# Kernel tuning notes

Hardware: AMD Instinct MI355X
Metric: run time of the kernel (lower is better)

## Reference

```python
import jax, jax.numpy as jnp
import numpy as np

B, T, U = 8, 200, 50
EPROJS = 512
DUNITS = 512
EMB = 512
JOINT = 512
ODIM = 1000
BLANK = 0


def setup_inputs() -> dict:
    key = jax.random.key(0)
    ks = jax.random.split(key, 16)
    s = lambda k, shape: (jax.random.normal(k, shape, jnp.float32) * 0.05)
    inp = {
        "hs_pad": jax.random.normal(ks[0], (B, T, EPROJS), jnp.float32),
        "ys_in_pad": jax.random.randint(ks[1], (B, U), 0, ODIM),
        "emb": s(ks[2], (ODIM, EMB)),
        "W_ih_0": s(ks[3], (4 * DUNITS, EMB)),
        "W_hh_0": s(ks[4], (4 * DUNITS, DUNITS)),
        "b_ih_0": s(ks[5], (4 * DUNITS,)),
        "b_hh_0": s(ks[6], (4 * DUNITS,)),
        "W_ih_1": s(ks[7], (4 * DUNITS, DUNITS)),
        "W_hh_1": s(ks[8], (4 * DUNITS, DUNITS)),
        "b_ih_1": s(ks[9], (4 * DUNITS,)),
        "b_hh_1": s(ks[10], (4 * DUNITS,)),
        "W_enc": s(ks[11], (JOINT, EPROJS)),
        "b_enc": s(ks[12], (JOINT,)),
        "W_dec": s(ks[13], (JOINT, DUNITS)),
        "W_out": s(ks[14], (ODIM, JOINT)),
        "b_out": s(ks[15], (ODIM,)),
    }
    return inp


def _lstm_cell(x, h, c, W_ih, W_hh, b_ih, b_hh):
    # torch.nn.LSTMCell, gate order i, f, g, o
    gates = x @ W_ih.T + b_ih + h @ W_hh.T + b_hh
    i, f, g, o = jnp.split(gates, 4, axis=-1)
    c_new = jax.nn.sigmoid(f) * c + jax.nn.sigmoid(i) * jnp.tanh(g)
    h_new = jax.nn.sigmoid(o) * jnp.tanh(c_new)
    return h_new, c_new


def reference(hs_pad, ys_in_pad, emb, W_ih_0, W_hh_0, b_ih_0, b_hh_0,
              W_ih_1, W_hh_1, b_ih_1, b_hh_1, W_enc, b_enc, W_dec,
              W_out, b_out):
    # embedding with padding_idx=blank -> blank row is zero
    emb_tbl = emb.at[BLANK].set(0.0)
    eys = emb_tbl[ys_in_pad]            # (B, U, EMB)

    def step(carry, ey):
        h0, c0, h1, c1 = carry
        h0, c0 = _lstm_cell(ey, h0, c0, W_ih_0, W_hh_0, b_ih_0, b_hh_0)
        h1, c1 = _lstm_cell(h0, h1, c1, W_ih_1, W_hh_1, b_ih_1, b_hh_1)
        return (h0, c0, h1, c1), h1

    z0 = jnp.zeros((hs_pad.shape[0], DUNITS), hs_pad.dtype)
    _, h_dec = jax.lax.scan(step, (z0, z0, z0, z0),
                            jnp.swapaxes(eys, 0, 1))   # (U, B, D)
    h_dec = jnp.swapaxes(h_dec, 0, 1)                  # (B, U, D)

    # joint: project first, then broadcast-add (avoids (B,T,U,Henc) expand)
    z_enc = hs_pad @ W_enc.T + b_enc                   # (B, T, J)
    z_dec = h_dec @ W_dec.T                            # (B, U, J), no bias
    z = jnp.tanh(z_enc[:, :, None, :] + z_dec[:, None, :, :])  # (B,T,U,J)
    return z @ W_out.T + b_out                         # (B, T, U, ODIM)
```

## Files before the change

kernel.cpp:

```cpp
#include <hip/hip_runtime.h>
#include <cstdint>
#include <cstddef>

#define Tsz 200
#define Usz 50
#define Kd  512
#define G4h 2048
#define OD  1000

typedef __attribute__((ext_vector_type(8))) short short8;
typedef __attribute__((ext_vector_type(4))) short s16x4;
typedef __attribute__((ext_vector_type(4))) float f32x4;

__device__ __forceinline__ unsigned short f2bf(float x) {
  union { float f; unsigned u; } v; v.f = x;
  unsigned r = v.u + 0x7FFFu + ((v.u >> 16) & 1u);
  return (unsigned short)(r >> 16);
}
__device__ __forceinline__ float bf2f(unsigned short h) {
  union { unsigned u; float f; } v; v.u = ((unsigned)h) << 16; return v.f;
}
__device__ __forceinline__ void splits(float w, short& hi, short& lo) {
  unsigned short h = f2bf(w);
  hi = (short)h;
  lo = (short)f2bf(w - bf2f(h));
}
__device__ __forceinline__ void split8(float4 f0, float4 f1, short8& hi, short8& lo) {
  float v[8] = {f0.x, f0.y, f0.z, f0.w, f1.x, f1.y, f1.z, f1.w};
  #pragma unroll
  for (int i = 0; i < 8; ++i) { short a, b2; splits(v[i], a, b2); hi[i] = a; lo[i] = b2; }
}
__device__ __forceinline__ float ftanh(float x) {
  float ax = fabsf(x);
  float t = __expf(-2.0f * ax);
  float r = (1.0f - t) / (1.0f + t);
  return copysignf(r, x);
}
__device__ __forceinline__ float sigf(float x) {
  return 1.0f / (1.0f + __expf(-x));
}
__device__ __forceinline__ void astore(unsigned* p, unsigned v) {
  __hip_atomic_store(p, v, __ATOMIC_RELAXED, __HIP_MEMORY_SCOPE_AGENT);
}
__device__ __forceinline__ void gload16(const void* g, void* l) {
  __builtin_amdgcn_global_load_lds(
      (const __attribute__((address_space(1))) void*)g,
      (__attribute__((address_space(3))) void*)l, 16, 0, 0);
}
__device__ __forceinline__ void aload4x4(const unsigned* p0, const unsigned* p1,
                                         const unsigned* p2, const unsigned* p3,
                                         uint4& r0, uint4& r1, uint4& r2, uint4& r3) {
  asm volatile(
      "global_load_dwordx4 %0, %4, off sc0 sc1\n\t"
      "global_load_dwordx4 %1, %5, off sc0 sc1\n\t"
      "global_load_dwordx4 %2, %6, off sc0 sc1\n\t"
      "global_load_dwordx4 %3, %7, off sc0 sc1\n\t"
      "s_waitcnt vmcnt(0)"
      : "=&v"(r0), "=&v"(r1), "=&v"(r2), "=&v"(r3)
      : "v"(p0), "v"(p1), "v"(p2), "v"(p3)
      : "memory");
}
__device__ __forceinline__ void aload8x4(const unsigned* p0, const unsigned* p1,
                                         const unsigned* p2, const unsigned* p3,
                                         const unsigned* q0, const unsigned* q1,
                                         const unsigned* q2, const unsigned* q3,
                                         uint4& r0, uint4& r1, uint4& r2, uint4& r3,
                                         uint4& s0, uint4& s1, uint4& s2, uint4& s3) {
  asm volatile(
      "global_load_dwordx4 %0, %8, off sc0 sc1\n\t"
      "global_load_dwordx4 %1, %9, off sc0 sc1\n\t"
      "global_load_dwordx4 %2, %10, off sc0 sc1\n\t"
      "global_load_dwordx4 %3, %11, off sc0 sc1\n\t"
      "global_load_dwordx4 %4, %12, off sc0 sc1\n\t"
      "global_load_dwordx4 %5, %13, off sc0 sc1\n\t"
      "global_load_dwordx4 %6, %14, off sc0 sc1\n\t"
      "global_load_dwordx4 %7, %15, off sc0 sc1\n\t"
      "s_waitcnt vmcnt(0)"
      : "=&v"(r0), "=&v"(r1), "=&v"(r2), "=&v"(r3),
        "=&v"(s0), "=&v"(s1), "=&v"(s2), "=&v"(s3)
      : "v"(p0), "v"(p1), "v"(p2), "v"(p3),
        "v"(q0), "v"(q1), "v"(q2), "v"(q3)
      : "memory");
}
__device__ __forceinline__ unsigned tagbad4(uint4 v, unsigned tg) {
  return ((v.x ^ tg) | (v.y ^ tg) | (v.z ^ tg) | (v.w ^ tg)) & 0xFFu;
}

__global__ __launch_bounds__(256) void k_prep(
    const int* __restrict__ ys, const float* __restrict__ emb,
    const float* __restrict__ Wih0, const float* __restrict__ bih0,
    const float* __restrict__ bhh0,
    unsigned* __restrict__ h0s, unsigned* __restrict__ h1s,
    float* __restrict__ xgr) {
  __shared__ float Al[16 * 516];
  __shared__ int idxs[16];
  const int bid = blockIdx.x;
  const int tid = threadIdx.x;

  if (bid < 16) {
    int i = bid * 256 + tid;
    if (i < 4096) { h0s[i] = 0u; h1s[i] = 0u; }
    return;
  }
  int q = bid - 16;
  int m0 = (q % 25) * 16;
  int n0 = (q / 25) * 64;
  if (tid < 16) {
    int m = m0 + tid;
    int u = m >> 3, b = m & 7;
    idxs[tid] = ys[b * Usz + u];
  }
  __syncthreads();
  for (int i = tid; i < 16 * 512; i += 256) {
    int r = i >> 9, k = i & 511;
    int idx = idxs[r];
    Al[r * 516 + k] = (idx == 0) ? 0.0f : emb[(size_t)idx * Kd + k];
  }
  __syncthreads();
  int nl = tid & 63;
  int mg = (tid >> 6) * 4;
  int n = n0 + nl;
  const float* Wr = Wih0 + (size_t)n * Kd;
  float acc[4] = {0.f, 0.f, 0.f, 0.f};
  #pragma unroll 4
  for (int k = 0; k < 512; k += 4) {
    float4 w = *(const float4*)(Wr + k);
    #pragma unroll
    for (int j = 0; j < 4; ++j) {
      const float* ar = &Al[(mg + j) * 516 + k];
      acc[j] += ar[0] * w.x + ar[1] * w.y + ar[2] * w.z + ar[3] * w.w;
    }
  }
  float bias = bih0[n] + bhh0[n];
  int g = n >> 9, jc = n & 511;
  #pragma unroll
  for (int j = 0; j < 4; ++j) {
    int m = m0 + mg + j;
    int u = m >> 3, b = m & 7;
    xgr[(((size_t)u * 32 + (jc >> 4)) * 4 + g) * 128 + (jc & 15) * 8 + b] =
        acc[j] + bias;
  }
}

__global__ __launch_bounds__(256) void k_gemm(const float* __restrict__ A,
                                              const float* __restrict__ W,
                                              float* __restrict__ C, int N) {
  __shared__ float Al[16 * 516];
  int m0 = blockIdx.x * 16;
  int n0 = blockIdx.y * 64;
  for (int i = threadIdx.x; i < 16 * 512; i += 256) {
    int r = i >> 9, k = i & 511;
    Al[r * 516 + k] = A[(size_t)(m0 + r) * Kd + k];
  }
  __syncthreads();
  int nl = threadIdx.x & 63;
  int mg = (threadIdx.x >> 6) * 4;
  int n = n0 + nl;
  const float* Wr = W + (size_t)n * Kd;
  float acc[4] = {0.f, 0.f, 0.f, 0.f};
  #pragma unroll 4
  for (int k = 0; k < 512; k += 4) {
    float4 w = *(const float4*)(Wr + k);
    #pragma unroll
    for (int j = 0; j < 4; ++j) {
      const float* ar = &Al[(mg + j) * 516 + k];
      acc[j] += ar[0] * w.x + ar[1] * w.y + ar[2] * w.z + ar[3] * w.w;
    }
  }
  #pragma unroll
  for (int j = 0; j < 4; ++j)
    C[(size_t)(m0 + mg + j) * N + n] = acc[j];
}

__global__ __launch_bounds__(256, 1) void k_lstm_zenc(
    const float* __restrict__ Whh0, const float* __restrict__ Wih1,
    const float* __restrict__ Whh1, const float* __restrict__ bih1,
    const float* __restrict__ bhh1, const float* __restrict__ xgr,
    unsigned* __restrict__ h0s, unsigned* __restrict__ h1s,
    float* __restrict__ hdec,
    const float* __restrict__ Wout, unsigned short* __restrict__ Wb,
    const float* __restrict__ hs, const float* __restrict__ Wenc,
    const float* __restrict__ benc, float* __restrict__ zenc) {
  __shared__ __align__(16) unsigned short sd[34816];
  unsigned short* H0H = sd;
  unsigned short* H0L = sd + 8192;
  unsigned short* H1H = sd + 16384;
  unsigned short* H1L = sd + 24576;
  float* gsm = (float*)(sd + 32768);

  const int tid = threadIdx.x;
  const int lane = tid & 63;
  const int wv = tid >> 6;
  const int bid = blockIdx.x;

  if (bid >= 352) {
    float* Al = (float*)sd;
    int q = bid - 352;
    int m0 = (q % 100) * 16;
    int n0 = (q / 100) * 64;
    for (int i = tid; i < 16 * 512; i += 256) {
      int r = i >> 9, k = i & 511;
      Al[r * 516 + k] = hs[(size_t)(m0 + r) * Kd + k];
    }
    __syncthreads();
    int nl = tid & 63;
    int mg = (tid >> 6) * 4;
    int n = n0 + nl;
    const float* Wr = Wenc + (size_t)n * Kd;
    float acc[4] = {0.f, 0.f, 0.f, 0.f};
    #pragma unroll 4
    for (int k = 0; k < 512; k += 4) {
      float4 w = *(const float4*)(Wr + k);
      #pragma unroll
      for (int j = 0; j < 4; ++j) {
        const float* ar = &Al[(mg + j) * 516 + k];
        acc[j] += ar[0] * w.x + ar[1] * w.y + ar[2] * w.z + ar[3] * w.w;
      }
    }
    float bias = benc[n];
    #pragma unroll
    for (int j = 0; j < 4; ++j)
      zenc[(size_t)(m0 + mg + j) * 512 + n] = acc[j] + bias;
    return;
  }
  if (bid >= 96) {
    int idx = (bid - 96) * 256 + tid;
    int n = idx >> 6, chunk = idx & 63;
    short8 v;
    if (n < OD) {
      const float* src = Wout + (size_t)n * Kd + chunk * 8;
      #pragma unroll
      for (int j = 0; j < 8; ++j) v[j] = (short)f2bf(src[j]);
    } else {
      #pragma unroll
      for (int j = 0; j < 8; ++j) v[j] = 0;
    }
    int tile = n >> 5, srow = n & 31;
    size_t off = (size_t)tile * 32768 + srow * 1024 +
                 ((chunk * 16) ^ ((srow & 7) << 4));
    *(short8*)((char*)Wb + off) = v;
    return;
  }

  const int kq = lane >> 4;
  const int cl = lane & 15;
  const int gg = (tid & 127) >> 1;
  const int sub = (tid & 1) << 3;
  const int swz = (gg & 7) << 4;
  const int gbase = gg << 8;
  const int tb = tid >> 7;

  if (bid < 32) {
    const int j0 = bid * 16;
    short8 whi[16], wlo[16];
    {
      const float* wr = Whh0 + ((size_t)(wv * 512 + j0 + cl)) * Kd;
      #pragma unroll
      for (int kt = 0; kt < 16; ++kt) {
        const float* p4 = wr + kt * 32 + kq * 8;
        split8(*(const float4*)p4, *(const float4*)(p4 + 4), whi[kt], wlo[kt]);
      }
    }
    float creg = 0.0f;
    const int ejl = tid & 15, eb = (tid >> 4) & 7;
    for (int p = 0; p < 50; ++p) {
      const float* xp = xgr + (((size_t)p * 32 + bid) * 4) * 128 + ejl * 8 + eb;
      float x0 = xp[0], x1 = xp[128], x2 = xp[256], x3 = xp[384];
      {
        const unsigned* bp = h0s + (size_t)p * 4096 + (tid << 2);
        uint4 v0, v1, v2, v3;
        aload4x4(bp, bp + 1024, bp + 2048, bp + 3072, v0, v1, v2, v3);
        const unsigned tg = (unsigned)p;
        for (int guard = 0; guard < (1 << 18); ++guard) {
          unsigned bad = tagbad4(v0, tg) | tagbad4(v1, tg) |
                         tagbad4(v2, tg) | tagbad4(v3, tg);
          if (!bad) break;
          __builtin_amdgcn_s_sleep(1);
          aload4x4(bp, bp + 1024, bp + 2048, bp + 3072, v0, v1, v2, v3);
        }
        unsigned uu[4][4] = {{v0.x, v0.y, v0.z, v0.w}, {v1.x, v1.y, v1.z, v1.w},
                             {v2.x, v2.y, v2.z, v2.w}, {v3.x, v3.y, v3.z, v3.w}};
        #pragma unroll
        for (int j = 0; j < 4; ++j) {
          s16x4 hv, lv;
          #pragma unroll
          for (int e = 0; e < 4; ++e) {
            short hh, ll; splits(__uint_as_float(uu[j][e]), hh, ll);
            hv[e] = hh; lv[e] = ll;
          }
          int b = j * 2 + tb;
          int off = gbase + (((b << 4) + sub) ^ swz);
          *(s16x4*)((char*)H0H + off) = hv;
          *(s16x4*)((char*)H0L + off) = lv;
        }
      }
      __syncthreads();
      f32x4 accA = {0.f, 0.f, 0.f, 0.f};
      f32x4 accB = {0.f, 0.f, 0.f, 0.f};
      f32x4 accC = {0.f, 0.f, 0.f, 0.f};
      #pragma unroll
      for (int kt = 0; kt < 16; ++kt) {
        int g = kt * 4 + kq;
        int off = (g << 8) + ((cl << 4) ^ ((g & 7) << 4));
        short8 bh = *(const short8*)((const char*)H0H + off);
        short8 bl = *(const short8*)((const char*)H0L + off);
        accA = __builtin_amdgcn_mfma_f32_16x16x32_bf16(whi[kt], bh, accA, 0, 0, 0);
        accB = __builtin_amdgcn_mfma_f32_16x16x32_bf16(wlo[kt], bh, accB, 0, 0, 0);
        accC = __builtin_amdgcn_mfma_f32_16x16x32_bf16(whi[kt], bl, accC, 0, 0, 0);
      }
      f32x4 acc = (accA + accB) + accC;
      *(f32x4*)&gsm[(wv * 16 + cl) * 16 + kq * 4] = acc;
      __syncthreads();
      if (tid < 128) {
        float g0 = gsm[(0 * 16 + eb) * 16 + ejl];
        float g1 = gsm[(1 * 16 + eb) * 16 + ejl];
        float g2 = gsm[(2 * 16 + eb) * 16 + ejl];
        float g3 = gsm[(3 * 16 + eb) * 16 + ejl];
        float gi = g0 + x0;
        float gf = g1 + x1;
        float gg2 = g2 + x2;
        float go = g3 + x3;
        float cn = sigf(gf) * creg + sigf(gi) * ftanh(gg2);
        float hn = sigf(go) * ftanh(cn);
        creg = cn;
        unsigned hv = (__float_as_uint(hn) & ~0xFFu) | (unsigned)(p + 1);
        astore(h0s + (size_t)(p + 1) * 4096 + eb * 512 + j0 + ejl, hv);
      }
      __syncthreads();
    }
  } else {
    const int j0 = (bid - 32) * 8;
    const int mt = wv & 1, kh = wv >> 1;
    short8 wihh[8], wihl[8], whhh[8], whhl[8];
    {
      const int g = mt * 2 + (cl >> 3), jl = cl & 7;
      const float* wr0 = Wih1 + ((size_t)(g * 512 + j0 + jl)) * Kd;
      const float* wr1 = Whh1 + ((size_t)(g * 512 + j0 + jl)) * Kd;
      #pragma unroll
      for (int k2 = 0; k2 < 8; ++k2) {
        int kt = kh * 8 + k2;
        const float* p0 = wr0 + kt * 32 + kq * 8;
        const float* p1 = wr1 + kt * 32 + kq * 8;
        split8(*(const float4*)p0, *(const float4*)(p0 + 4), wihh[k2], wihl[k2]);
        split8(*(const float4*)p1, *(const float4*)(p1 + 4), whhh[k2], whhl[k2]);
      }
    }
    float creg = 0.0f;
    const int ejl = tid & 7, eb = (tid >> 3) & 7;
    float bs0 = bih1[0 * 512 + j0 + ejl] + bhh1[0 * 512 + j0 + ejl];
    float bs1 = bih1[1 * 512 + j0 + ejl] + bhh1[1 * 512 + j0 + ejl];
    float bs2 = bih1[2 * 512 + j0 + ejl] + bhh1[2 * 512 + j0 + ejl];
    float bs3 = bih1[3 * 512 + j0 + ejl] + bhh1[3 * 512 + j0 + ejl];
    for (int p = 1; p <= 50; ++p) {
      {
        const unsigned* bp0 = h0s + (size_t)p * 4096 + (tid << 2);
        const unsigned* bp1 = h1s + (size_t)(p - 1) * 4096 + (tid << 2);
        uint4 v0, v1, v2, v3, w0, w1, w2, w3;
        aload8x4(bp0, bp0 + 1024, bp0 + 2048, bp0 + 3072,
                 bp1, bp1 + 1024, bp1 + 2048, bp1 + 3072,
                 v0, v1, v2, v3, w0, w1, w2, w3);
        const unsigned tg0 = (unsigned)p, tg1 = (unsigned)(p - 1);
        for (int guard = 0; guard < (1 << 18); ++guard) {
          unsigned bad = tagbad4(v0, tg0) | tagbad4(v1, tg0) |
                         tagbad4(v2, tg0) | tagbad4(v3, tg0) |
                         tagbad4(w0, tg1) | tagbad4(w1, tg1) |
                         tagbad4(w2, tg1) | tagbad4(w3, tg1);
          if (!bad) break;
          __builtin_amdgcn_s_sleep(1);
          aload8x4(bp0, bp0 + 1024, bp0 + 2048, bp0 + 3072,
                   bp1, bp1 + 1024, bp1 + 2048, bp1 + 3072,
                   v0, v1, v2, v3, w0, w1, w2, w3);
        }
        unsigned uu[4][4] = {{v0.x, v0.y, v0.z, v0.w}, {v1.x, v1.y, v1.z, v1.w},
                             {v2.x, v2.y, v2.z, v2.w}, {v3.x, v3.y, v3.z, v3.w}};
        unsigned tt[4][4] = {{w0.x, w0.y, w0.z, w0.w}, {w1.x, w1.y, w1.z, w1.w},
                             {w2.x, w2.y, w2.z, w2.w}, {w3.x, w3.y, w3.z, w3.w}};
        #pragma unroll
        for (int j = 0; j < 4; ++j) {
          s16x4 hv, lv, hw, lw;
          #pragma unroll
          for (int e = 0; e < 4; ++e) {
            short hh, ll;
            splits(__uint_as_float(uu[j][e]), hh, ll); hv[e] = hh; lv[e] = ll;
            splits(__uint_as_float(tt[j][e]), hh, ll); hw[e] = hh; lw[e] = ll;
          }
          int b = j * 2 + tb;
          int off = gbase + (((b << 4) + sub) ^ swz);
          *(s16x4*)((char*)H0H + off) = hv;
          *(s16x4*)((char*)H0L + off) = lv;
          *(s16x4*)((char*)H1H + off) = hw;
          *(s16x4*)((char*)H1L + off) = lw;
        }
      }
      __syncthreads();
      f32x4 q0 = {0.f,0.f,0.f,0.f}, q1 = {0.f,0.f,0.f,0.f}, q2 = {0.f,0.f,0.f,0.f};
      f32x4 q3 = {0.f,0.f,0.f,0.f}, q4 = {0.f,0.f,0.f,0.f}, q5 = {0.f,0.f,0.f,0.f};
      #pragma unroll
      for (int k2 = 0; k2 < 8; ++k2) {
        int kt = kh * 8 + k2;
        int g = kt * 4 + kq;
        int off = (g << 8) + ((cl << 4) ^ ((g & 7) << 4));
        short8 b0h = *(const short8*)((const char*)H0H + off);
        short8 b0l = *(const short8*)((const char*)H0L + off);
        short8 b1h = *(const short8*)((const char*)H1H + off);
        short8 b1l = *(const short8*)((const char*)H1L + off);
        q0 = __builtin_amdgcn_mfma_f32_16x16x32_bf16(wihh[k2], b0h, q0, 0, 0, 0);
        q1 = __builtin_amdgcn_mfma_f32_16x16x32_bf16(wihl[k2], b0h, q1, 0, 0, 0);
        q2 = __builtin_amdgcn_mfma_f32_16x16x32_bf16(wihh[k2], b0l, q2, 0, 0, 0);
        q3 = __builtin_amdgcn_mfma_f32_16x16x32_bf16(whhh[k2], b1h, q3, 0, 0, 0);
        q4 = __builtin_amdgcn_mfma_f32_16x16x32_bf16(whhl[k2], b1h, q4, 0, 0, 0);
        q5 = __builtin_amdgcn_mfma_f32_16x16x32_bf16(whhh[k2], b1l, q5, 0, 0, 0);
      }
      f32x4 acc = ((q0 + q1) + (q2 + q3)) + (q4 + q5);
      *(f32x4*)&gsm[(wv * 16 + cl) * 16 + kq * 4] = acc;
      __syncthreads();
      if (tid < 64) {
        float gv[4];
        #pragma unroll
        for (int g = 0; g < 4; ++g) {
          int mtg = g >> 1, r = (g & 1) * 8 + ejl;
          gv[g] = gsm[(mtg * 16 + eb) * 16 + r] + gsm[((2 + mtg) * 16 + eb) * 16 + r];
        }
        float gi = gv[0] + bs0, gf = gv[1] + bs1, gg2 = gv[2] + bs2, go = gv[3] + bs3;
        float cn = sigf(gf) * creg + sigf(gi) * ftanh(gg2);
        float hn = sigf(go) * ftanh(cn);
        creg = cn;
        int jg = j0 + ejl;
        unsigned hv = (__float_as_uint(hn) & ~0xFFu) | (unsigned)p;
        astore(h1s + (size_t)p * 4096 + eb * 512 + jg, hv);
        hdec[((size_t)eb * Usz + (p - 1)) * Kd + jg] = __uint_as_float(hv);
      }
      __syncthreads();
    }
  }
}

__global__ __launch_bounds__(256) void k_joint(const float* __restrict__ zenc,
                                               const float* __restrict__ zdec,
                                               const unsigned short* __restrict__ Wb,
                                               const float* __restrict__ bout,
                                               float* __restrict__ out) {
  __shared__ __align__(16) unsigned short Blds[2 * 16384];
  const int lane = threadIdx.x & 63;
  const int wv = threadIdx.x >> 6;
  const int kgrp = lane >> 4;
  const int rl = lane & 15;
  const int rbase = blockIdx.x * 64 + wv * 16;

  short8 a[16];
  {
    int row = rbase + rl;
    int u = row % Usz;
    int bt = row / Usz;
    const float* ze = zenc + (size_t)bt * Kd;
    const float* zd = zdec + (size_t)((bt / Tsz) * Usz + u) * Kd;
    #pragma unroll
    for (int kk = 0; kk < 16; ++kk) {
      int k0 = kk * 32 + kgrp * 8;
      float4 e0 = *(const float4*)(ze + k0);
      float4 e1 = *(const float4*)(ze + k0 + 4);
      float4 d0 = *(const float4*)(zd + k0);
      float4 d1 = *(const float4*)(zd + k0 + 4);
      short8 tt;
      tt[0] = (short)f2bf(ftanh(e0.x + d0.x));
      tt[1] = (short)f2bf(ftanh(e0.y + d0.y));
      tt[2] = (short)f2bf(ftanh(e0.z + d0.z));
      tt[3] = (short)f2bf(ftanh(e0.w + d0.w));
      tt[4] = (short)f2bf(ftanh(e1.x + d1.x));
      tt[5] = (short)f2bf(ftanh(e1.y + d1.y));
      tt[6] = (short)f2bf(ftanh(e1.z + d1.z));
      tt[7] = (short)f2bf(ftanh(e1.w + d1.w));
      a[kk] = tt;
    }
  }

  #pragma unroll
  for (int i = 0; i < 8; ++i) {
    int o = (i * 4 + wv) * 1024;
    gload16((const char*)Wb + o + lane * 16, (char*)Blds + o);
  }
  asm volatile("s_waitcnt vmcnt(0)" ::: "memory");
  __builtin_amdgcn_s_barrier();
  __builtin_amdgcn_sched_barrier(0);

  int cur = 0;
  for (int it = 0; it < 32; ++it) {
    if (it < 31) {
      const char* g = (const char*)Wb + (size_t)(it + 1) * 32768;
      char* l = (char*)Blds + (cur ^ 1) * 32768;
      #pragma unroll
      for (int i = 0; i < 8; ++i) {
        int o = (i * 4 + wv) * 1024;
        gload16(g + o + lane * 16, l + o);
      }
      __builtin_amdgcn_sched_barrier(0);
    }
    const char* bufc = (const char*)Blds + cur * 32768;
    int n0 = it * 32;
    f32x4 acc0 = {0.f, 0.f, 0.f, 0.f};
    f32x4 acc1 = {0.f, 0.f, 0.f, 0.f};
    #pragma unroll
    for (int kk = 0; kk < 16; ++kk) {
      int c = kk * 4 + kgrp;
      int b0 = ((c * 16) ^ ((rl & 7) << 4)) + rl * 1024;
      int b1 = ((c * 16) ^ ((rl & 7) << 4)) + (rl + 16) * 1024;
      short8 bf0 = *(const short8*)(bufc + b0);
      short8 bf1 = *(const short8*)(bufc + b1);
      acc0 = __builtin_amdgcn_mfma_f32_16x16x32_bf16(a[kk], bf0, acc0, 0, 0, 0);
      acc1 = __builtin_amdgcn_mfma_f32_16x16x32_bf16(a[kk], bf1, acc1, 0, 0, 0);
    }
    #pragma unroll
    for (int nt = 0; nt < 2; ++nt) {
      int n = n0 + nt * 16 + rl;
      if (n < OD) {
        float bo = bout[n];
        const f32x4& A0 = nt ? acc1 : acc0;
        size_t r0 = (size_t)(rbase + kgrp * 4) * OD + n;
        #pragma unroll
        for (int j = 0; j < 4; ++j)
          out[r0 + (size_t)j * OD] = A0[j] + bo;
      }
    }
    if (it < 31) {
      __builtin_amdgcn_sched_barrier(0);
      asm volatile("s_waitcnt vmcnt(8)" ::: "memory");
      __builtin_amdgcn_s_barrier();
      __builtin_amdgcn_sched_barrier(0);
    }
    cur ^= 1;
  }
}

extern "C" void kernel_launch(void* const* d_in, const int* in_sizes, int n_in,
                              void* d_out, int out_size, void* d_ws, size_t ws_size,
                              hipStream_t stream) {
  const float* hs   = (const float*)d_in[0];
  const int*   ys   = (const int*)d_in[1];
  const float* emb  = (const float*)d_in[2];
  const float* Wih0 = (const float*)d_in[3];
  const float* Whh0 = (const float*)d_in[4];
  const float* bih0 = (const float*)d_in[5];
  const float* bhh0 = (const float*)d_in[6];
  const float* Wih1 = (const float*)d_in[7];
  const float* Whh1 = (const float*)d_in[8];
  const float* bih1 = (const float*)d_in[9];
  const float* bhh1 = (const float*)d_in[10];
  const float* Wenc = (const float*)d_in[11];
  const float* benc = (const float*)d_in[12];
  const float* Wdec = (const float*)d_in[13];
  const float* Wout = (const float*)d_in[14];
  const float* bout = (const float*)d_in[15];
  float* out = (float*)d_out;

  float* ws   = (float*)d_ws;
  float* xgr  = ws + 204800;
  float* zenc = ws + 1024000;
  float* zdec = ws + 1843200;
  float* hdec = ws + 2048000;
  unsigned short* Wb = (unsigned short*)(ws + 2252800);
  unsigned* h0s = (unsigned*)(ws + 2514944);
  unsigned* h1s = (unsigned*)(ws + 2723840);

  k_prep<<<816, 256, 0, stream>>>(ys, emb, Wih0, bih0, bhh0, h0s, h1s, xgr);
  k_lstm_zenc<<<1152, 256, 0, stream>>>(Whh0, Wih1, Whh1, bih1, bhh1, xgr,
                                        h0s, h1s, hdec, Wout, Wb,
                                        hs, Wenc, benc, zenc);
  k_gemm<<<dim3(25, 8), 256, 0, stream>>>(hdec, Wdec, zdec, 512);
  k_joint<<<1250, 256, 0, stream>>>(zenc, zdec, Wb, bout, out);
}
```

Baseline: 373.4 us.

## Fuse decoder projection into LSTM kernel via per-step flag-polling blocks

Removes the separate z_dec GEMM launch and the hdec buffer. The LSTM kernel gains 200 extra blocks, one per (step u, 128-column quarter). Each polls the tagged h1 state for its step, copies it to LDS, and computes z_dec rows for all batches while the recurrence continues. This hides the decoder projection behind the serial LSTM and drops a launch. The risk is that spin-waiting blocks take CU slots, or get scheduled before the producer blocks and stall.

```diff
diff --git a/kernel.cpp b/kernel.cpp
--- a/kernel.cpp
+++ b/kernel.cpp
@@ -85,6 +85,9 @@
 __device__ __forceinline__ unsigned tagbad4(uint4 v, unsigned tg) {
   return ((v.x ^ tg) | (v.y ^ tg) | (v.z ^ tg) | (v.w ^ tg)) & 0xFFu;
 }
+__device__ __forceinline__ void bsleep(int slp) {
+  for (int s = 0; s < slp; ++s) __builtin_amdgcn_s_sleep(16);
+}
 
 __global__ __launch_bounds__(256) void k_prep(
     const int* __restrict__ ys, const float* __restrict__ emb,
@@ -142,45 +145,15 @@
   }
 }
 
-__global__ __launch_bounds__(256) void k_gemm(const float* __restrict__ A,
-                                              const float* __restrict__ W,
-                                              float* __restrict__ C, int N) {
-  __shared__ float Al[16 * 516];
-  int m0 = blockIdx.x * 16;
-  int n0 = blockIdx.y * 64;
-  for (int i = threadIdx.x; i < 16 * 512; i += 256) {
-    int r = i >> 9, k = i & 511;
-    Al[r * 516 + k] = A[(size_t)(m0 + r) * Kd + k];
-  }
-  __syncthreads();
-  int nl = threadIdx.x & 63;
-  int mg = (threadIdx.x >> 6) * 4;
-  int n = n0 + nl;
-  const float* Wr = W + (size_t)n * Kd;
-  float acc[4] = {0.f, 0.f, 0.f, 0.f};
-  #pragma unroll 4
-  for (int k = 0; k < 512; k += 4) {
-    float4 w = *(const float4*)(Wr + k);
-    #pragma unroll
-    for (int j = 0; j < 4; ++j) {
-      const float* ar = &Al[(mg + j) * 516 + k];
-      acc[j] += ar[0] * w.x + ar[1] * w.y + ar[2] * w.z + ar[3] * w.w;
-    }
-  }
-  #pragma unroll
-  for (int j = 0; j < 4; ++j)
-    C[(size_t)(m0 + mg + j) * N + n] = acc[j];
-}
-
 __global__ __launch_bounds__(256, 1) void k_lstm_zenc(
     const float* __restrict__ Whh0, const float* __restrict__ Wih1,
     const float* __restrict__ Whh1, const float* __restrict__ bih1,
     const float* __restrict__ bhh1, const float* __restrict__ xgr,
     unsigned* __restrict__ h0s, unsigned* __restrict__ h1s,
-    float* __restrict__ hdec,
     const float* __restrict__ Wout, unsigned short* __restrict__ Wb,
     const float* __restrict__ hs, const float* __restrict__ Wenc,
-    const float* __restrict__ benc, float* __restrict__ zenc) {
+    const float* __restrict__ benc, float* __restrict__ zenc,
+    const float* __restrict__ Wdec, float* __restrict__ zdec) {
   __shared__ __align__(16) unsigned short sd[34816];
   unsigned short* H0H = sd;
   unsigned short* H0L = sd + 8192;
@@ -193,6 +166,51 @@
   const int wv = tid >> 6;
   const int bid = blockIdx.x;
 
+  if (bid >= 1152) {
+    float* hl = (float*)sd;
+    const int q2 = bid - 1152;
+    const int u = q2 >> 2;
+    const int nq = q2 & 3;
+    const int p = u + 1;
+    {
+      const unsigned* bp = h1s + (size_t)p * 4096 + tid * 16;
+      uint4 v0, v1, v2, v3;
+      aload4x4(bp, bp + 4, bp + 8, bp + 12, v0, v1, v2, v3);
+      const unsigned tg = (unsigned)p & 0xFFu;
+      int slp = 1;
+      for (int guard = 0; guard < (1 << 14); ++guard) {
+        unsigned bad = tagbad4(v0, tg) | tagbad4(v1, tg) |
+                       tagbad4(v2, tg) | tagbad4(v3, tg);
+        if (!bad) break;
+        bsleep(slp);
+        if (slp < 8) slp <<= 1;
+        aload4x4(bp, bp + 4, bp + 8, bp + 12, v0, v1, v2, v3);
+      }
+      *(uint4*)&hl[tid * 16] = v0;
+      *(uint4*)&hl[tid * 16 + 4] = v1;
+      *(uint4*)&hl[tid * 16 + 8] = v2;
+      *(uint4*)&hl[tid * 16 + 12] = v3;
+    }
+    __syncthreads();
+    if (tid < 128) {
+      int n = nq * 128 + tid;
+      const float* wp = Wdec + (size_t)n * Kd;
+      float acc[8] = {0, 0, 0, 0, 0, 0, 0, 0};
+      #pragma unroll 4
+      for (int kc = 0; kc < 128; ++kc) {
+        float4 w = *(const float4*)(wp + kc * 4);
+        #pragma unroll
+        for (int b = 0; b < 8; ++b) {
+          float4 h4 = *(const float4*)&hl[b * 512 + kc * 4];
+          acc[b] += w.x * h4.x + w.y * h4.y + w.z * h4.z + w.w * h4.w;
+        }
+      }
+      #pragma unroll
+      for (int b = 0; b < 8; ++b)
+        zdec[((size_t)(b * Usz + u) << 9) + n] = acc[b];
+    }
+    return;
+  }
   if (bid >= 352) {
     float* Al = (float*)sd;
     int q = bid - 352;
@@ -428,7 +446,6 @@
         int jg = j0 + ejl;
         unsigned hv = (__float_as_uint(hn) & ~0xFFu) | (unsigned)p;
         astore(h1s + (size_t)p * 4096 + eb * 512 + jg, hv);
-        hdec[((size_t)eb * Usz + (p - 1)) * Kd + jg] = __uint_as_float(hv);
       }
       __syncthreads();
     }
@@ -556,15 +573,13 @@
   float* xgr  = ws + 204800;
   float* zenc = ws + 1024000;
   float* zdec = ws + 1843200;
-  float* hdec = ws + 2048000;
   unsigned short* Wb = (unsigned short*)(ws + 2252800);
   unsigned* h0s = (unsigned*)(ws + 2514944);
   unsigned* h1s = (unsigned*)(ws + 2723840);
 
   k_prep<<<816, 256, 0, stream>>>(ys, emb, Wih0, bih0, bhh0, h0s, h1s, xgr);
-  k_lstm_zenc<<<1152, 256, 0, stream>>>(Whh0, Wih1, Whh1, bih1, bhh1, xgr,
-                                        h0s, h1s, hdec, Wout, Wb,
-                                        hs, Wenc, benc, zenc);
-  k_gemm<<<dim3(25, 8), 256, 0, stream>>>(hdec, Wdec, zdec, 512);
+  k_lstm_zenc<<<1352, 256, 0, stream>>>(Whh0, Wih1, Whh1, bih1, bhh1, xgr,
+                                        h0s, h1s, Wout, Wb,
+                                        hs, Wenc, benc, zenc, Wdec, zdec);
   k_joint<<<1250, 256, 0, stream>>>(zenc, zdec, Wb, bout, out);
 }
```

Result: faster. 355.3 us (-4.8%).
